# Kernel tuning notes

Hardware: AMD Instinct MI355X
Metric: run time of the kernel (lower is better)

## Reference

```python
import jax, jax.numpy as jnp
import numpy as np

VARIANCE = (0.1, 0.2)
THRESHOLD = 0.5
NEG_POS = 3


def point_form(boxes):
    # (cx,cy,w,h) -> (xmin,ymin,xmax,ymax)
    return jnp.concatenate([boxes[:, :2] - boxes[:, 2:] / 2,
                            boxes[:, :2] + boxes[:, 2:] / 2], axis=1)


def jaccard(a, b):
    # a: [T,4] xyxy truths, b: [P,4] xyxy priors -> IoU [T,P]
    lt = jnp.maximum(a[:, None, :2], b[None, :, :2])
    rb = jnp.minimum(a[:, None, 2:], b[None, :, 2:])
    wh = jnp.clip(rb - lt, 0.0)
    inter = wh[..., 0] * wh[..., 1]
    area_a = ((a[:, 2] - a[:, 0]) * (a[:, 3] - a[:, 1]))[:, None]
    area_b = ((b[:, 2] - b[:, 0]) * (b[:, 3] - b[:, 1]))[None, :]
    return inter / (area_a + area_b - inter)


def encode(matched, priors):
    g_cxcy = (matched[:, :2] + matched[:, 2:]) / 2 - priors[:, :2]
    g_cxcy = g_cxcy / (VARIANCE[0] * priors[:, 2:])
    g_wh = jnp.log((matched[:, 2:] - matched[:, :2]) / priors[:, 2:]) / VARIANCE[1]
    return jnp.concatenate([g_cxcy, g_wh], axis=1)


def match_one(truths, priors):
    # SSD match for one image; labels are zeroed in BiBoxLoss -> binary conf {0,1}
    overlaps = jaccard(truths, point_form(priors))          # [T,P]
    best_prior_idx = jnp.argmax(overlaps, axis=1)           # [T]
    best_truth_overlap = jnp.max(overlaps, axis=0)          # [P]
    best_truth_idx = jnp.argmax(overlaps, axis=0)           # [P]
    best_truth_overlap = best_truth_overlap.at[best_prior_idx].set(2.0)
    best_truth_idx = best_truth_idx.at[best_prior_idx].set(
        jnp.arange(truths.shape[0]))
    matched = truths[best_truth_idx]                        # [P,4]
    conf = jnp.where(best_truth_overlap < THRESHOLD, 0, 1)  # [P] int
    loc = encode(matched, priors)
    return loc, conf


def bibox_loss(loc_data, conf_data, priors, targets):
    num, num_priors = loc_data.shape[0], loc_data.shape[1]
    truths = targets[..., :4]                               # [B,T,4]
    loc_t, conf_t = jax.vmap(lambda t: match_one(t, priors))(truths)

    pos = conf_t > 0                                        # [B,P]
    # smooth L1 (sum) over positive priors
    ad = jnp.abs(loc_data - loc_t)
    sl1 = jnp.where(ad < 1.0, 0.5 * ad * ad, ad - 0.5)
    loss_l = jnp.sum(sl1 * pos[..., None].astype(loc_data.dtype))

    # per-prior CE (logsumexp - gathered logit) for hard-negative mining
    lse = jax.nn.logsumexp(conf_data, axis=-1)              # [B,P]
    gathered = jnp.take_along_axis(conf_data, conf_t[..., None], axis=-1)[..., 0]
    loss_c_all = lse - gathered                             # [B,P]

    loss_c_mine = jnp.where(pos, 0.0, loss_c_all)
    loss_idx = jnp.argsort(-loss_c_mine, axis=1)
    idx_rank = jnp.argsort(loss_idx, axis=1)                # rank of each prior
    num_pos = jnp.sum(pos.astype(jnp.int32), axis=1, keepdims=True)  # [B,1]
    num_neg = jnp.minimum(NEG_POS * num_pos, num_priors - 1)
    neg = idx_rank < num_neg                                # [B,P]

    sel = pos | neg
    loss_c = jnp.sum(jnp.where(sel, loss_c_all, 0.0))

    N = jnp.sum(num_pos).astype(loc_data.dtype)
    return loss_l / N, loss_c / N


def setup_inputs() -> dict:
    key = jax.random.key(0)
    k1, k2, k3, k4, k5, k6 = jax.random.split(key, 6)
    B, P, T = 32, 65536, 16
    loc_data = jax.random.normal(k1, (B, P, 4), dtype=jnp.float32)
    conf_data = jax.random.normal(k2, (B, P, 2), dtype=jnp.float32)
    # priors: valid center-form boxes
    pc = 0.15 + 0.7 * jax.random.uniform(k3, (P, 2), dtype=jnp.float32)
    pwh = 0.05 + 0.25 * jax.random.uniform(k4, (P, 2), dtype=jnp.float32)
    priors = jnp.concatenate([pc, pwh], axis=1)
    # targets: valid corner-form boxes + dummy label column (zeroed by the loss)
    tc = 0.2 + 0.6 * jax.random.uniform(k5, (B, T, 2), dtype=jnp.float32)
    twh = 0.05 + 0.25 * jax.random.uniform(k6, (B, T, 2), dtype=jnp.float32)
    boxes = jnp.concatenate([tc - twh / 2, tc + twh / 2], axis=-1)
    targets = jnp.concatenate(
        [boxes, jnp.ones((B, T, 1), dtype=jnp.float32)], axis=-1)
    return {"loc_data": loc_data, "conf_data": conf_data,
            "priors": priors, "targets": targets}


def reference(loc_data, conf_data, priors, targets):
    return bibox_loss(loc_data, conf_data, priors, targets)
```

## Files before the change

### kernel.cpp

```cpp
#include <hip/hip_runtime.h>

#define NB_ 32
#define NP_ 65536
#define NT_ 16
#define HB 1024
#define HSCALE 128.0f
#define NBX 32
#define CHUNKS 2

__device__ __forceinline__ float softplus_(float x) {
    return fmaxf(x, 0.0f) + __logf(1.0f + __expf(-fabsf(x)));
}

__device__ __forceinline__ float iou_fast(float tx0, float ty0, float tx1, float ty1, float ta,
                                          float bx0, float by0, float bx1, float by1, float ar) {
    float lx = fmaxf(tx0, bx0), ly = fmaxf(ty0, by0);
    float rx = fminf(tx1, bx1), ry = fminf(ty1, by1);
    float w = fmaxf(rx - lx, 0.0f), h = fmaxf(ry - ly, 0.0f);
    float inter = w * h;
    return __fdividef(inter, ta + ar - inter);
}

__global__ void __launch_bounds__(256) mainK(
    const float* __restrict__ loc, const float* __restrict__ conf,
    const float* __restrict__ priors, const float* __restrict__ targets,
    int* __restrict__ gcnt, float* __restrict__ gsum,
    unsigned long long* __restrict__ bestPart,
    float* __restrict__ part_ll, float* __restrict__ part_pc, int* __restrict__ part_np,
    unsigned* __restrict__ ticket)
{
    const int bx = blockIdx.x, b = blockIdx.y, tid = threadIdx.x;

    __shared__ float tr[NT_][5];
    __shared__ int hc[HB];
    __shared__ float hs[HB];
    __shared__ unsigned wkey[4][NT_], wp[4][NT_];
    __shared__ float sh_ll[4], sh_pc[4];
    __shared__ int sh_np[4];

    if (b == 0 && bx == 0 && tid == 0) *ticket = 0u;

    for (int i = tid; i < HB; i += 256) { hc[i] = 0; hs[i] = 0.0f; }
    if (tid < NT_) {
        const float* tp = targets + ((size_t)b * NT_ + tid) * 5;
        float x0 = tp[0], y0 = tp[1], x1 = tp[2], y1 = tp[3];
        tr[tid][0] = x0; tr[tid][1] = y0; tr[tid][2] = x1; tr[tid][3] = y1;
        tr[tid][4] = (x1 - x0) * (y1 - y0);
    }
    __syncthreads();

    float ll_acc = 0.0f, pc_acc = 0.0f;
    int np_acc = 0;
    unsigned tkey[NT_];
#pragma unroll
    for (int t = 0; t < NT_; t++) tkey[t] = 0u;

    for (int c = 0; c < CHUNKS; c++) {
        const int pbase = (bx * CHUNKS + c) * 1024 + tid;
        float4 pr[4];
        float pbx0[4], pby0[4], pbx1[4], pby1[4], par[4];
#pragma unroll
        for (int i = 0; i < 4; i++) {
            pr[i] = ((const float4*)priors)[pbase + 256 * i];
            float hw = pr[i].z * 0.5f, hh = pr[i].w * 0.5f;
            pbx0[i] = pr[i].x - hw; pby0[i] = pr[i].y - hh;
            pbx1[i] = pr[i].x + hw; pby1[i] = pr[i].y + hh;
            par[i] = (pbx1[i] - pbx0[i]) * (pby1[i] - pby0[i]);
        }
        unsigned pkey[4] = {0u, 0u, 0u, 0u};
#pragma unroll
        for (int t = 0; t < NT_; t++) {
            float tx0 = tr[t][0], ty0 = tr[t][1], tx1 = tr[t][2], ty1 = tr[t][3], ta = tr[t][4];
            unsigned lowt = (unsigned)(15 - t);
            unsigned lowc = (unsigned)(15 - c * 4);
#pragma unroll
            for (int i = 0; i < 4; i++) {
                float iou = iou_fast(tx0, ty0, tx1, ty1, ta,
                                     pbx0[i], pby0[i], pbx1[i], pby1[i], par[i]);
                unsigned base = (__float_as_uint(iou) & 0xFFFFFFFCu) << 2;
                unsigned kt = base | lowt;
                unsigned kp = base | (lowc - (unsigned)i);
                pkey[i] = (kt > pkey[i]) ? kt : pkey[i];
                tkey[t] = (kp > tkey[t]) ? kp : tkey[t];
            }
        }
#pragma unroll
        for (int i = 0; i < 4; i++) {
            int p = pbase + 256 * i;
            size_t bp = (size_t)b * NP_ + p;
            bool pos = (pkey[i] >= 0xFC000000u);
            float2 cxy = ((const float2*)conf)[bp];
            float dd = cxy.y - cxy.x;
            float v = pos ? 0.0f : softplus_(dd);
            int bin = min(HB - 1, (int)(v * HSCALE));
            atomicAdd(&hc[bin], 1);
            atomicAdd(&hs[bin], v);
            if (pos) {
                np_acc++;
                pc_acc += softplus_(-dd);
                int t = 15 - (int)(pkey[i] & 15u);
                float tx0 = tr[t][0], ty0 = tr[t][1], tx1 = tr[t][2], ty1 = tr[t][3];
                float gcx = ((tx0 + tx1) * 0.5f - pr[i].x) / (0.1f * pr[i].z);
                float gcy = ((ty0 + ty1) * 0.5f - pr[i].y) / (0.1f * pr[i].w);
                float gw = __logf((tx1 - tx0) / pr[i].z) * 5.0f;
                float gh = __logf((ty1 - ty0) / pr[i].w) * 5.0f;
                float4 ld = ((const float4*)loc)[bp];
                float d0 = fabsf(ld.x - gcx), d1 = fabsf(ld.y - gcy);
                float d2 = fabsf(ld.z - gw),  d3 = fabsf(ld.w - gh);
                ll_acc += (d0 < 1.0f) ? 0.5f * d0 * d0 : d0 - 0.5f;
                ll_acc += (d1 < 1.0f) ? 0.5f * d1 * d1 : d1 - 0.5f;
                ll_acc += (d2 < 1.0f) ? 0.5f * d2 * d2 : d2 - 0.5f;
                ll_acc += (d3 < 1.0f) ? 0.5f * d3 * d3 : d3 - 0.5f;
            }
        }
    }

    const int wave = tid >> 6, lane = tid & 63;
#pragma unroll
    for (int t = 0; t < NT_; t++) {
        unsigned k = tkey[t], m = k;
        for (int off = 32; off > 0; off >>= 1) {
            unsigned o = __shfl_down(m, off, 64);
            m = (o > m) ? o : m;
        }
        m = __shfl(m, 0, 64);
        unsigned long long ball = __ballot(k == m);
        if (lane == 0) {
            int l = __ffsll((long long)ball) - 1;
            int ci = 15 - (int)(m & 15u);
            int p = bx * (CHUNKS * 1024) + ci * 256 + wave * 64 + l;
            wkey[wave][t] = m;
            wp[wave][t] = (unsigned)p;
        }
    }
    for (int off = 32; off > 0; off >>= 1) {
        ll_acc += __shfl_down(ll_acc, off, 64);
        pc_acc += __shfl_down(pc_acc, off, 64);
        np_acc += __shfl_down(np_acc, off, 64);
    }
    if (lane == 0) { sh_ll[wave] = ll_acc; sh_pc[wave] = pc_acc; sh_np[wave] = np_acc; }
    __syncthreads();

    if (tid < NT_) {
        unsigned bk = wkey[0][tid], bpv = wp[0][tid];
        for (int w = 1; w < 4; w++) {
            unsigned k2 = wkey[w][tid], p2 = wp[w][tid];
            if (k2 > bk || (k2 == bk && p2 < bpv)) { bk = k2; bpv = p2; }
        }
        unsigned long long pk = (((unsigned long long)bk) << 32) | (unsigned)(~bpv);
        bestPart[((size_t)b * NT_ + tid) * NBX + bx] = pk;
    }
    if (tid == 0) {
        part_ll[b * NBX + bx] = sh_ll[0] + sh_ll[1] + sh_ll[2] + sh_ll[3];
        part_pc[b * NBX + bx] = sh_pc[0] + sh_pc[1] + sh_pc[2] + sh_pc[3];
        part_np[b * NBX + bx] = sh_np[0] + sh_np[1] + sh_np[2] + sh_np[3];
    }
    int* gc = gcnt + ((size_t)(b * NBX + bx)) * HB;
    float* gs = gsum + ((size_t)(b * NBX + bx)) * HB;
    for (int i = tid; i < HB; i += 256) { gc[i] = hc[i]; gs[i] = hs[i]; }
}

__global__ void __launch_bounds__(1024) finishK(
    const float* __restrict__ loc, const float* __restrict__ conf,
    const float* __restrict__ priors, const float* __restrict__ targets,
    const int* __restrict__ gcnt, const float* __restrict__ gsum,
    const unsigned long long* __restrict__ bestPart,
    const float* __restrict__ part_ll, const float* __restrict__ part_pc,
    const int* __restrict__ part_np,
    float* __restrict__ final_l, float* __restrict__ final_c, int* __restrict__ final_n,
    unsigned* __restrict__ ticket, float* __restrict__ out)
{
    const int b = blockIdx.x, tid = threadIdx.x;
    __shared__ int hc[HB];
    __shared__ float hs[HB];
    __shared__ float tr[NT_][5];
    __shared__ unsigned ps[NT_];
    __shared__ float s_dll, s_dpc;
    __shared__ int s_dnp;
    __shared__ unsigned ccnt[16];
    __shared__ float csm[16];
    __shared__ int s_last;

    if (tid == 0) { s_dll = 0.0f; s_dpc = 0.0f; s_dnp = 0; s_last = 0; }
    if (tid < NT_) {
        const float* tp = targets + ((size_t)b * NT_ + tid) * 5;
        float x0 = tp[0], y0 = tp[1], x1 = tp[2], y1 = tp[3];
        tr[tid][0] = x0; tr[tid][1] = y0; tr[tid][2] = x1; tr[tid][3] = y1;
        tr[tid][4] = (x1 - x0) * (y1 - y0);
    }
    {
        int i = tid;
        int c = 0; float s = 0.0f;
#pragma unroll
        for (int j = 0; j < NBX; j++) {
            c += gcnt[((size_t)(b * NBX + j)) * HB + i];
            s += gsum[((size_t)(b * NBX + j)) * HB + i];
        }
        hc[i] = c; hs[i] = s;
    }
    if (tid < NT_) {
        unsigned long long v = bestPart[((size_t)b * NT_ + tid) * NBX];
        for (int j = 1; j < NBX; j++) {
            unsigned long long u = bestPart[((size_t)b * NT_ + tid) * NBX + j];
            if (u > v) v = u;
        }
        ps[tid] = ~((unsigned)(v & 0xffffffffULL));
    }
    __syncthreads();

    if (tid < NT_) {
        unsigned p = ps[tid];
        bool active = true;
        for (int u = tid + 1; u < NT_; u++)
            if (ps[u] == p) { active = false; break; }
        if (active) {
            float4 prv = ((const float4*)priors)[p];
            float hw = prv.z * 0.5f, hh = prv.w * 0.5f;
            float qx0 = prv.x - hw, qy0 = prv.y - hh;
            float qx1 = prv.x + hw, qy1 = prv.y + hh;
            float areab = (qx1 - qx0) * (qy1 - qy0);
            unsigned pk = 0u;
            for (int tt = 0; tt < NT_; tt++) {
                float iou = iou_fast(tr[tt][0], tr[tt][1], tr[tt][2], tr[tt][3], tr[tt][4],
                                     qx0, qy0, qx1, qy1, areab);
                unsigned cand = ((__float_as_uint(iou) & 0xFFFFFFFCu) << 2)
                              | (unsigned)(15 - tt);
                pk = (cand > pk) ? cand : pk;
            }
            bool pos0 = (pk >= 0xFC000000u);
            int t0 = 15 - (int)(pk & 15u);
            size_t bp = (size_t)b * NP_ + p;
            float2 cxy = ((const float2*)conf)[bp];
            float dd = cxy.y - cxy.x;
            float4 ld = ((const float4*)loc)[bp];

            auto sl1_of = [&](int tt) -> float {
                float tx0 = tr[tt][0], ty0 = tr[tt][1], tx1 = tr[tt][2], ty1 = tr[tt][3];
                float gcx = ((tx0 + tx1) * 0.5f - prv.x) / (0.1f * prv.z);
                float gcy = ((ty0 + ty1) * 0.5f - prv.y) / (0.1f * prv.w);
                float gw = __logf((tx1 - tx0) / prv.z) * 5.0f;
                float gh = __logf((ty1 - ty0) / prv.w) * 5.0f;
                float d0 = fabsf(ld.x - gcx), d1 = fabsf(ld.y - gcy);
                float d2 = fabsf(ld.z - gw),  d3 = fabsf(ld.w - gh);
                float s = (d0 < 1.0f) ? 0.5f * d0 * d0 : d0 - 0.5f;
                s += (d1 < 1.0f) ? 0.5f * d1 * d1 : d1 - 0.5f;
                s += (d2 < 1.0f) ? 0.5f * d2 * d2 : d2 - 0.5f;
                s += (d3 < 1.0f) ? 0.5f * d3 * d3 : d3 - 0.5f;
                return s;
            };
            float dll = sl1_of(tid) - (pos0 ? sl1_of(t0) : 0.0f);
            atomicAdd(&s_dll, dll);
            if (!pos0) {
                float v = softplus_(dd);
                int bin = min(HB - 1, (int)(v * HSCALE));
                atomicSub(&hc[bin], 1);
                atomicAdd(&hs[bin], -v);
                atomicAdd(&s_dpc, softplus_(-dd));
                atomicAdd(&s_dnp, 1);
            }
        }
    }
    __syncthreads();

    if (tid < 16) {
        unsigned cacc = 0; float sacc = 0.0f;
        for (int j = 0; j < 64; j++) { cacc += (unsigned)hc[tid * 64 + j]; sacc += hs[tid * 64 + j]; }
        ccnt[tid] = cacc; csm[tid] = sacc;
    }
    __syncthreads();

    if (tid == 0) {
        float sll = s_dll, spc = s_dpc;
        int n = s_dnp;
        for (int j = 0; j < NBX; j++) {
            sll += part_ll[b * NBX + j];
            spc += part_pc[b * NBX + j];
            n += part_np[b * NBX + j];
        }
        int K = 3 * n;
        if (K > NP_ - 1) K = NP_ - 1;
        float tk = 0.0f;
        if (K > 0) {
            unsigned need = (unsigned)K, cum = 0;
            float s = 0.0f;
            int cb = 15;
            for (; cb > 0; --cb) {
                if (cum + ccnt[cb] >= need) break;
                cum += ccnt[cb]; s += csm[cb];
            }
            int bin = cb * 64 + 63;
            for (; bin > cb * 64; --bin) {
                if (cum + (unsigned)hc[bin] >= need) break;
                cum += (unsigned)hc[bin]; s += hs[bin];
            }
            unsigned rem = need - cum;
            int cv = hc[bin];
            float avg = (cv > 0) ? __fdividef(hs[bin], (float)cv) : 0.0f;
            tk = s + (float)rem * avg;
        }
        final_l[b] = sll;
        final_c[b] = spc + tk;
        final_n[b] = n;
        __threadfence();
        unsigned old = atomicAdd(ticket, 1u);
        if (old == NB_ - 1) s_last = 1;
    }
    __syncthreads();

    if (s_last) {
        __threadfence();
        if (tid < 64) {
            float lv = 0.0f, cv = 0.0f;
            int nv = 0;
            if (tid < NB_) { lv = final_l[tid]; cv = final_c[tid]; nv = final_n[tid]; }
            for (int off = 32; off > 0; off >>= 1) {
                lv += __shfl_down(lv, off, 64);
                cv += __shfl_down(cv, off, 64);
                nv += __shfl_down(nv, off, 64);
            }
            if (tid == 0) {
                float fn = (float)nv;
                out[0] = lv / fn;
                out[1] = cv / fn;
            }
        }
    }
}

extern "C" void kernel_launch(void* const* d_in, const int* in_sizes, int n_in,
                              void* d_out, int out_size, void* d_ws, size_t ws_size,
                              hipStream_t stream) {
    const float* loc = (const float*)d_in[0];
    const float* conf = (const float*)d_in[1];
    const float* priors = (const float*)d_in[2];
    const float* targets = (const float*)d_in[3];
    float* out = (float*)d_out;

    char* w = (char*)d_ws;
    int* gcnt = (int*)w;
    float* gsum = (float*)(w + (4u << 20));
    char* acc = w + (8u << 20);
    unsigned long long* bestPart = (unsigned long long*)acc;
    float* part_ll = (float*)(acc + (128u << 10));
    float* part_pc = (float*)(acc + (128u << 10) + 4096);
    int* part_np   = (int*)(acc + (128u << 10) + 8192);
    float* final_l = (float*)(acc + (128u << 10) + 12288);
    float* final_c = (float*)(acc + (128u << 10) + 12416);
    int* final_n   = (int*)(acc + (128u << 10) + 12544);
    unsigned* ticket = (unsigned*)(acc + (128u << 10) + 12672);

    mainK<<<dim3(NBX, NB_), 256, 0, stream>>>(loc, conf, priors, targets,
                                              gcnt, gsum, bestPart,
                                              part_ll, part_pc, part_np, ticket);
    finishK<<<NB_, 1024, 0, stream>>>(loc, conf, priors, targets, gcnt, gsum, bestPart,
                                      part_ll, part_pc, part_np,
                                      final_l, final_c, final_n, ticket, out);
}
```

Baseline: 149.3 us.

## Fuse per-image finish pass into main kernel via last-block ticket

Removes the separate finishK launch. The last mainK block to finish for each image, detected with a per-image atomic ticket, merges the partial histograms and best-prior parts, and a global ticket picks the block that writes the final output. Ticket counters are now zeroed with a hipMemsetAsync before the launch. This saves the second kernel's launch and gap, but the merge now runs on 256 threads instead of 1024 and adds a memset operation.

```diff
diff --git a/kernel.cpp b/kernel.cpp
--- a/kernel.cpp
+++ b/kernel.cpp
@@ -27,7 +27,9 @@
     int* __restrict__ gcnt, float* __restrict__ gsum,
     unsigned long long* __restrict__ bestPart,
     float* __restrict__ part_ll, float* __restrict__ part_pc, int* __restrict__ part_np,
-    unsigned* __restrict__ ticket)
+    float* __restrict__ final_l, float* __restrict__ final_c, int* __restrict__ final_n,
+    unsigned* __restrict__ bticket, unsigned* __restrict__ gticket,
+    float* __restrict__ out)
 {
     const int bx = blockIdx.x, b = blockIdx.y, tid = threadIdx.x;
 
@@ -37,8 +39,12 @@
     __shared__ unsigned wkey[4][NT_], wp[4][NT_];
     __shared__ float sh_ll[4], sh_pc[4];
     __shared__ int sh_np[4];
-
-    if (b == 0 && bx == 0 && tid == 0) *ticket = 0u;
+    __shared__ unsigned ps[NT_];
+    __shared__ float s_dll, s_dpc;
+    __shared__ int s_dnp;
+    __shared__ unsigned ccnt[16];
+    __shared__ float csm[16];
+    __shared__ int s_merge, s_lastg;
 
     for (int i = tid; i < HB; i += 256) { hc[i] = 0; hs[i] = 0.0f; }
     if (tid < NT_) {
@@ -155,43 +161,27 @@
         part_pc[b * NBX + bx] = sh_pc[0] + sh_pc[1] + sh_pc[2] + sh_pc[3];
         part_np[b * NBX + bx] = sh_np[0] + sh_np[1] + sh_np[2] + sh_np[3];
     }
-    int* gc = gcnt + ((size_t)(b * NBX + bx)) * HB;
-    float* gs = gsum + ((size_t)(b * NBX + bx)) * HB;
-    for (int i = tid; i < HB; i += 256) { gc[i] = hc[i]; gs[i] = hs[i]; }
-}
-
-__global__ void __launch_bounds__(1024) finishK(
-    const float* __restrict__ loc, const float* __restrict__ conf,
-    const float* __restrict__ priors, const float* __restrict__ targets,
-    const int* __restrict__ gcnt, const float* __restrict__ gsum,
-    const unsigned long long* __restrict__ bestPart,
-    const float* __restrict__ part_ll, const float* __restrict__ part_pc,
-    const int* __restrict__ part_np,
-    float* __restrict__ final_l, float* __restrict__ final_c, int* __restrict__ final_n,
-    unsigned* __restrict__ ticket, float* __restrict__ out)
-{
-    const int b = blockIdx.x, tid = threadIdx.x;
-    __shared__ int hc[HB];
-    __shared__ float hs[HB];
-    __shared__ float tr[NT_][5];
-    __shared__ unsigned ps[NT_];
-    __shared__ float s_dll, s_dpc;
-    __shared__ int s_dnp;
-    __shared__ unsigned ccnt[16];
-    __shared__ float csm[16];
-    __shared__ int s_last;
-
-    if (tid == 0) { s_dll = 0.0f; s_dpc = 0.0f; s_dnp = 0; s_last = 0; }
-    if (tid < NT_) {
-        const float* tp = targets + ((size_t)b * NT_ + tid) * 5;
-        float x0 = tp[0], y0 = tp[1], x1 = tp[2], y1 = tp[3];
-        tr[tid][0] = x0; tr[tid][1] = y0; tr[tid][2] = x1; tr[tid][3] = y1;
-        tr[tid][4] = (x1 - x0) * (y1 - y0);
-    }
     {
-        int i = tid;
+        int* gc = gcnt + ((size_t)(b * NBX + bx)) * HB;
+        float* gs = gsum + ((size_t)(b * NBX + bx)) * HB;
+        for (int i = tid; i < HB; i += 256) { gc[i] = hc[i]; gs[i] = hs[i]; }
+    }
+
+    __threadfence();
+    __syncthreads();
+    if (tid == 0) {
+        unsigned old = atomicAdd(&bticket[b], 1u);
+        s_merge = (old == NBX - 1) ? 1 : 0;
+        s_dll = 0.0f; s_dpc = 0.0f; s_dnp = 0; s_lastg = 0;
+    }
+    __syncthreads();
+    if (!s_merge) return;
+    __threadfence();
+
+#pragma unroll
+    for (int k = 0; k < 4; k++) {
+        int i = k * 256 + tid;
         int c = 0; float s = 0.0f;
-#pragma unroll
         for (int j = 0; j < NBX; j++) {
             c += gcnt[((size_t)(b * NBX + j)) * HB + i];
             s += gsum[((size_t)(b * NBX + j)) * HB + i];
@@ -302,12 +292,12 @@
         final_c[b] = spc + tk;
         final_n[b] = n;
         __threadfence();
-        unsigned old = atomicAdd(ticket, 1u);
-        if (old == NB_ - 1) s_last = 1;
-    }
-    __syncthreads();
-
-    if (s_last) {
+        unsigned old = atomicAdd(gticket, 1u);
+        if (old == NB_ - 1) s_lastg = 1;
+    }
+    __syncthreads();
+
+    if (s_lastg) {
         __threadfence();
         if (tid < 64) {
             float lv = 0.0f, cv = 0.0f;
@@ -347,12 +337,13 @@
     float* final_l = (float*)(acc + (128u << 10) + 12288);
     float* final_c = (float*)(acc + (128u << 10) + 12416);
     int* final_n   = (int*)(acc + (128u << 10) + 12544);
-    unsigned* ticket = (unsigned*)(acc + (128u << 10) + 12672);
-
+    unsigned* bticket = (unsigned*)(acc + (128u << 10) + 12672);
+    unsigned* gticket = (unsigned*)(acc + (128u << 10) + 12800);
+
+    hipMemsetAsync(bticket, 0, 132, stream);
     mainK<<<dim3(NBX, NB_), 256, 0, stream>>>(loc, conf, priors, targets,
                                               gcnt, gsum, bestPart,
-                                              part_ll, part_pc, part_np, ticket);
-    finishK<<<NB_, 1024, 0, stream>>>(loc, conf, priors, targets, gcnt, gsum, bestPart,
-                                      part_ll, part_pc, part_np,
-                                      final_l, final_c, final_n, ticket, out);
+                                              part_ll, part_pc, part_np,
+                                              final_l, final_c, final_n,
+                                              bticket, gticket, out);
 }
```

New measurement: 261.7 us. 75.3% more time.
